# Kernel optimization log

Hardware: AMD Instinct MI355X
Metric: run time of the kernel (lower is better)

Reference implementation:

```python
import jax, jax.numpy as jnp
import numpy as np

B, H, W = 8, 64, 64
DIM_RGB, DIM_PL, EMBED, OUT = 256, 256, 128, 256
BN_EPS = 1e-5


def conv1x1(x, w, b=None):
    # x: (B,C,H,W), w: (D,C) -> (B,D,H,W)
    y = jnp.einsum('bchw,dc->bdhw', x, w)
    if b is not None:
        y = y + b[None, :, None, None]
    return y


def spatial_attention(q, k, v, scale):
    # q,k,v: (B,D,H,W)
    b, d, h, w = q.shape
    n = h * w
    qf = q.reshape(b, d, n).transpose(0, 2, 1)   # (B,N,D)
    kf = k.reshape(b, d, n)                       # (B,D,N)
    vf = v.reshape(b, d, n).transpose(0, 2, 1)   # (B,N,D)
    attn = jax.nn.softmax(jnp.einsum('bnd,bdm->bnm', qf, kf) * scale, axis=-1)
    out = jnp.einsum('bnm,bmd->bnd', attn, vf)   # (B,N,D)
    return out.transpose(0, 2, 1).reshape(b, d, h, w)


def setup_inputs() -> dict:
    key = jax.random.key(0)
    ks = jax.random.split(key, 20)
    s = 0.05
    inp = {
        'f_rgb': jax.random.normal(ks[0], (B, DIM_RGB, H, W), jnp.float32),
        'f_pl': jax.random.normal(ks[1], (B, DIM_PL, H, W), jnp.float32),
        'w_q_rgb': jax.random.normal(ks[2], (EMBED, DIM_RGB), jnp.float32) * s,
        'b_q_rgb': jax.random.normal(ks[3], (EMBED,), jnp.float32) * s,
        'w_k_pl': jax.random.normal(ks[4], (EMBED, DIM_PL), jnp.float32) * s,
        'b_k_pl': jax.random.normal(ks[5], (EMBED,), jnp.float32) * s,
        'w_v_pl': jax.random.normal(ks[6], (EMBED, DIM_PL), jnp.float32) * s,
        'b_v_pl': jax.random.normal(ks[7], (EMBED,), jnp.float32) * s,
        'w_q_pl': jax.random.normal(ks[8], (EMBED, DIM_PL), jnp.float32) * s,
        'b_q_pl': jax.random.normal(ks[9], (EMBED,), jnp.float32) * s,
        'w_k_rgb': jax.random.normal(ks[10], (EMBED, DIM_RGB), jnp.float32) * s,
        'b_k_rgb': jax.random.normal(ks[11], (EMBED,), jnp.float32) * s,
        'w_v_rgb': jax.random.normal(ks[12], (EMBED, DIM_RGB), jnp.float32) * s,
        'b_v_rgb': jax.random.normal(ks[13], (EMBED,), jnp.float32) * s,
        'w_proj': jax.random.normal(ks[14], (OUT, 2 * EMBED), jnp.float32) * s,
        'bn_gamma': jnp.ones((OUT,), jnp.float32),
        'bn_beta': jnp.zeros((OUT,), jnp.float32),
        'bn_mean': jax.random.normal(ks[15], (OUT,), jnp.float32) * 0.01,
        'bn_var': jax.random.uniform(ks[16], (OUT,), jnp.float32, 0.5, 1.5),
    }
    return inp


def reference(f_rgb, f_pl, w_q_rgb, b_q_rgb, w_k_pl, b_k_pl, w_v_pl, b_v_pl,
              w_q_pl, b_q_pl, w_k_rgb, b_k_rgb, w_v_rgb, b_v_rgb,
              w_proj, bn_gamma, bn_beta, bn_mean, bn_var):
    scale = EMBED ** -0.5
    out_rgb2pl = spatial_attention(
        conv1x1(f_rgb, w_q_rgb, b_q_rgb),
        conv1x1(f_pl, w_k_pl, b_k_pl),
        conv1x1(f_pl, w_v_pl, b_v_pl), scale)
    out_pl2rgb = spatial_attention(
        conv1x1(f_pl, w_q_pl, b_q_pl),
        conv1x1(f_rgb, w_k_rgb, b_k_rgb),
        conv1x1(f_rgb, w_v_rgb, b_v_rgb), scale)
    combined = jnp.concatenate([out_rgb2pl, out_pl2rgb], axis=1)  # (B,2E,H,W)
    y = conv1x1(combined, w_proj)  # no bias
    # BatchNorm2d (inference form) + ReLU
    inv = bn_gamma * jax.lax.rsqrt(bn_var + BN_EPS)
    y = y * inv[None, :, None, None] + (bn_beta - bn_mean * inv)[None, :, None, None]
    return jax.nn.relu(y)
```

## Files before the change

kernel.cpp:

```cpp
#include <hip/hip_runtime.h>
#include <hip/hip_bf16.h>
#include <hip/hip_fp16.h>

typedef _Float16 f16;
typedef _Float16 f16x8 __attribute__((ext_vector_type(8)));
typedef _Float16 f16x4 __attribute__((ext_vector_type(4)));
typedef __fp16 hf16x2 __attribute__((ext_vector_type(2)));
typedef float f32x4 __attribute__((ext_vector_type(4)));
typedef float f32x16 __attribute__((ext_vector_type(16)));

#define NP   4096
#define NB   8
#define CINC 256
#define EMB  128
#define OUTC 256
#define BN_EPS 1e-5f

#define DSZ  ((size_t)NB * NP * EMB)
#define TSZ  (2 * DSZ)

__global__ __launch_bounds__(256) void proj_all_kernel(
    const float* __restrict__ Xrgb, const float* __restrict__ Xpl,
    const float* __restrict__ w0, const float* __restrict__ b0,
    const float* __restrict__ w1, const float* __restrict__ b1,
    const float* __restrict__ w2, const float* __restrict__ b2,
    const float* __restrict__ w3, const float* __restrict__ b3,
    const float* __restrict__ w4, const float* __restrict__ b4,
    const float* __restrict__ w5, const float* __restrict__ b5,
    f16* __restrict__ Qt, f16* __restrict__ Kt, f16* __restrict__ Vn)
{
    const int m0 = blockIdx.x * 128;
    const int p  = blockIdx.y;
    const int b  = blockIdx.z;
    const int s  = (p >= 3) ? 1 : 0;
    const int j  = p - s * 3;
    const int tid = threadIdx.x;
    const int w = tid >> 6, lane = tid & 63, quad = lane >> 4, lr = lane & 15;

    const float* X  = s ? Xpl : Xrgb;
    const float* W  = p == 0 ? w0 : p == 1 ? w1 : p == 2 ? w2
                    : p == 3 ? w3 : p == 4 ? w4 : w5;
    const float* Bi = p == 0 ? b0 : p == 1 ? b1 : p == 2 ? b2
                    : p == 3 ? b3 : p == 4 ? b4 : b5;

    __shared__ __align__(16) f16 smem[128 * 72 * 2];
    f16* Al = smem;
    f16* Bl = smem + 128 * 72;

    f32x4 acc[2][8];
    #pragma unroll
    for (int mi = 0; mi < 2; ++mi)
        #pragma unroll
        for (int ni = 0; ni < 8; ++ni) acc[mi][ni] = (f32x4){0.f, 0.f, 0.f, 0.f};

    for (int kt = 0; kt < 4; ++kt) {
        const int kc0 = kt * 64;
        __syncthreads();
        for (int s2 = tid; s2 < 1024; s2 += 256) {
            const int n = s2 & 127, cg = s2 >> 7;
            f16 tmp[8];
            #pragma unroll
            for (int jj = 0; jj < 8; ++jj)
                tmp[jj] = (f16)X[((size_t)b * CINC + kc0 + cg * 8 + jj) * NP + m0 + n];
            *(f16x8*)&Al[n * 72 + cg * 8] = *(const f16x8*)tmp;
        }
        for (int s2 = tid; s2 < 1024; s2 += 256) {
            const int d = s2 >> 3, cg = s2 & 7;
            f16 tmp[8];
            #pragma unroll
            for (int jj = 0; jj < 8; ++jj)
                tmp[jj] = (f16)W[(size_t)d * CINC + kc0 + cg * 8 + jj];
            *(f16x8*)&Bl[d * 72 + cg * 8] = *(const f16x8*)tmp;
        }
        __syncthreads();
        #pragma unroll
        for (int ks = 0; ks < 2; ++ks) {
            f16x8 af[2], bfr[8];
            #pragma unroll
            for (int mi = 0; mi < 2; ++mi)
                af[mi] = *(const f16x8*)&Al[(w * 32 + mi * 16 + lr) * 72 + ks * 32 + quad * 8];
            #pragma unroll
            for (int ni = 0; ni < 8; ++ni)
                bfr[ni] = *(const f16x8*)&Bl[(ni * 16 + lr) * 72 + ks * 32 + quad * 8];
            #pragma unroll
            for (int mi = 0; mi < 2; ++mi)
                #pragma unroll
                for (int ni = 0; ni < 8; ++ni)
                    acc[mi][ni] = __builtin_amdgcn_mfma_f32_16x16x32_f16(
                        af[mi], bfr[ni], acc[mi][ni], 0, 0, 0);
        }
    }

    float bias[8];
    #pragma unroll
    for (int ni = 0; ni < 8; ++ni) bias[ni] = Bi[ni * 16 + lr];

    if (j < 2) {
        f16* out = (j == 0) ? (Qt + (size_t)s * DSZ) : (Kt + (size_t)(1 - s) * DSZ);
        #pragma unroll
        for (int mi = 0; mi < 2; ++mi)
            #pragma unroll
            for (int ni = 0; ni < 8; ++ni)
                #pragma unroll
                for (int r = 0; r < 4; ++r) {
                    const int n = m0 + w * 32 + mi * 16 + quad * 4 + r;
                    out[((size_t)b * NP + n) * EMB + ni * 16 + lr] =
                        (f16)(acc[mi][ni][r] + bias[ni]);
                }
    } else {
        f16* outV = Vn + (size_t)(1 - s) * DSZ;
        __syncthreads();
        f16* T = smem;
        const int quad_p = ((quad & 1) << 1) | (quad >> 1);
        #pragma unroll
        for (int mi = 0; mi < 2; ++mi)
            #pragma unroll
            for (int ni = 0; ni < 8; ++ni)
                #pragma unroll
                for (int r = 0; r < 4; ++r)
                    T[(ni * 16 + lr) * 136 + w * 32 + mi * 16 + quad_p * 4 + r] =
                        (f16)(acc[mi][ni][r] + bias[ni]);
        __syncthreads();
        for (int s2 = tid; s2 < 2048; s2 += 256) {
            const int d = s2 >> 4, n8 = (s2 & 15) * 8;
            *(f16x8*)&outV[((size_t)b * EMB + d) * NP + m0 + n8] =
                *(const f16x8*)&T[d * 136 + n8];
        }
    }
}

__global__ __launch_bounds__(256, 2) void attn_kernel(
    const f16* __restrict__ Qt, const f16* __restrict__ Kt,
    const f16* __restrict__ Vn, f16* __restrict__ combT)
{
    const int bid = blockIdx.x;
    const int g = bid & 15, dir = g >> 3, b = g & 7;
    const int n0 = (bid >> 4) * 128;
    const int tid = threadIdx.x;
    const int w = tid >> 6, lane = tid & 63;
    const int l31 = lane & 31, hi = lane >> 5;

    const f16* __restrict__ Q = Qt + ((size_t)dir * NB + b) * NP * EMB;
    const f16* __restrict__ K = Kt + ((size_t)dir * NB + b) * NP * EMB;
    const f16* __restrict__ V = Vn + ((size_t)dir * NB + b) * (size_t)EMB * NP;

    __shared__ __align__(16) f16 Kl[2][64 * 128];
    __shared__ __align__(16) f16 Vl[2][128 * 64];

    const int qbase = n0 + w * 32;

    f16x8 qf[8];
    #pragma unroll
    for (int d16 = 0; d16 < 8; ++d16) {
        f16x8 q = *(const f16x8*)&Q[(size_t)(qbase + l31) * EMB + d16 * 16 + hi * 8];
        #pragma unroll
        for (int jj = 0; jj < 8; ++jj)
            q[jj] = q[jj] * (f16)0.12752749f;
        qf[d16] = q;
    }

    f32x16 O[4];
    #pragma unroll
    for (int d32 = 0; d32 < 4; ++d32) O[d32] = (f32x16)(0.0f);
    float rs = 0.f;

    const int krp = lane >> 4, kp = lane & 15;
    const int vrp = lane >> 3, vp = lane & 7;
    f16x8 stK[4], stV[4];

    auto stage_load = [&](int m0) {
        #pragma unroll
        for (int i = 0; i < 4; ++i) {
            const int r = w * 16 + i * 4 + krp;
            const int c = kp ^ (r & 7);
            stK[i] = *(const f16x8*)&K[(size_t)(m0 + r) * EMB + c * 8];
        }
        #pragma unroll
        for (int i = 0; i < 4; ++i) {
            const int r = w * 32 + i * 8 + vrp;
            const int c = vp ^ (r & 7);
            stV[i] = *(const f16x8*)&V[(size_t)r * NP + m0 + c * 8];
        }
    };
    auto stage_write = [&](int buf) {
        #pragma unroll
        for (int i = 0; i < 4; ++i) {
            const int r = w * 16 + i * 4 + krp;
            *(f16x8*)&Kl[buf][r * 128 + kp * 8] = stK[i];
        }
        #pragma unroll
        for (int i = 0; i < 4; ++i) {
            const int r = w * 32 + i * 8 + vrp;
            *(f16x8*)&Vl[buf][r * 64 + vp * 8] = stV[i];
        }
    };

    stage_load(0);
    stage_write(0);
    int cur = 0;

    for (int t = 0; t < NP / 64; ++t) {
        __syncthreads();
        if (t < NP / 64 - 1) stage_load((t + 1) * 64);

        const f16* Kb = &Kl[cur][0];
        const f16* Vb = &Vl[cur][0];

        #pragma unroll
        for (int k32 = 0; k32 < 2; ++k32) {
            f32x16 s = (f32x16)(0.0f);
            __builtin_amdgcn_s_setprio(1);
            #pragma unroll
            for (int d16 = 0; d16 < 8; ++d16) {
                const int r = k32 * 32 + l31;
                const int c = (d16 * 2 + hi) ^ (r & 7);
                const f16x8 kf = *(const f16x8*)&Kb[r * 128 + c * 8];
                s = __builtin_amdgcn_mfma_f32_32x32x16_f16(kf, qf[d16], s, 0, 0, 0);
            }
            __builtin_amdgcn_s_setprio(0);

            float e[16];
            #pragma unroll
            for (int i = 0; i < 16; ++i) e[i] = __builtin_amdgcn_exp2f(s[i]);
            float sum = 0.f;
            #pragma unroll
            for (int i = 0; i < 16; ++i) sum += e[i];
            rs += sum;
            f16x8 pb[2];
            #pragma unroll
            for (int g2 = 0; g2 < 2; ++g2) {
                union { hf16x2 h[4]; f16x8 v; } pu;
                #pragma unroll
                for (int t2 = 0; t2 < 4; ++t2)
                    pu.h[t2] = __builtin_amdgcn_cvt_pkrtz(e[g2 * 8 + t2 * 2],
                                                          e[g2 * 8 + t2 * 2 + 1]);
                pb[g2] = pu.v;
            }

            __builtin_amdgcn_s_setprio(1);
            #pragma unroll
            for (int g2 = 0; g2 < 2; ++g2) {
                #pragma unroll
                for (int d32 = 0; d32 < 4; ++d32) {
                    const int r = d32 * 32 + l31;
                    const int c = (k32 * 4 + g2 * 2 + hi) ^ (r & 7);
                    const f16x8 vf = *(const f16x8*)&Vb[r * 64 + c * 8];
                    O[d32] = __builtin_amdgcn_mfma_f32_32x32x16_f16(vf, pb[g2], O[d32], 0, 0, 0);
                }
            }
            __builtin_amdgcn_s_setprio(0);
        }

        if (t < NP / 64 - 1) stage_write(cur ^ 1);
        cur ^= 1;
    }

    rs += __shfl_xor(rs, 32);
    const float inv = 1.0f / rs;
    const int n = qbase + l31;
    #pragma unroll
    for (int d32 = 0; d32 < 4; ++d32)
        #pragma unroll
        for (int tq = 0; tq < 4; ++tq) {
            f16 o4[4];
            #pragma unroll
            for (int jj = 0; jj < 4; ++jj)
                o4[jj] = (f16)(O[d32][tq * 4 + jj] * inv);
            *(f16x4*)&combT[((size_t)b * NP + n) * OUTC + dir * EMB + d32 * 32 + tq * 8 + hi * 4] =
                *(const f16x4*)o4;
        }
}

__global__ __launch_bounds__(256) void proj_out_kernel(
    const f16* __restrict__ combT, const float* __restrict__ Wp,
    const float* __restrict__ G, const float* __restrict__ Be,
    const float* __restrict__ Mu, const float* __restrict__ Va,
    float* __restrict__ out)
{
    const int m0 = blockIdx.x * 128;
    const int o0 = blockIdx.y * 128;
    const int b  = blockIdx.z;
    const int tid = threadIdx.x;
    const int w = tid >> 6, lane = tid & 63, quad = lane >> 4, lr = lane & 15;

    __shared__ __align__(16) f16 smem[128 * 72 * 2];
    f16* Al = smem;
    f16* Bl = smem + 128 * 72;

    f32x4 acc[2][8];
    #pragma unroll
    for (int mi = 0; mi < 2; ++mi)
        #pragma unroll
        for (int ni = 0; ni < 8; ++ni) acc[mi][ni] = (f32x4){0.f, 0.f, 0.f, 0.f};

    for (int kt = 0; kt < 4; ++kt) {
        const int kc0 = kt * 64;
        __syncthreads();
        #pragma unroll
        for (int i = 0; i < 4; ++i) {
            const int s2 = i * 256 + tid;
            const int n = s2 >> 3, cg = s2 & 7;
            *(f16x8*)&Al[n * 72 + cg * 8] =
                *(const f16x8*)&combT[((size_t)b * NP + m0 + n) * OUTC + kc0 + cg * 8];
        }
        for (int s2 = tid; s2 < 1024; s2 += 256) {
            const int d = s2 >> 3, cg = s2 & 7;
            f16 tmp[8];
            #pragma unroll
            for (int jj = 0; jj < 8; ++jj)
                tmp[jj] = (f16)Wp[(size_t)(o0 + d) * OUTC + kc0 + cg * 8 + jj];
            *(f16x8*)&Bl[d * 72 + cg * 8] = *(const f16x8*)tmp;
        }
        __syncthreads();
        #pragma unroll
        for (int ks = 0; ks < 2; ++ks) {
            f16x8 af[2], bfr[8];
            #pragma unroll
            for (int mi = 0; mi < 2; ++mi)
                af[mi] = *(const f16x8*)&Al[(w * 32 + mi * 16 + lr) * 72 + ks * 32 + quad * 8];
            #pragma unroll
            for (int ni = 0; ni < 8; ++ni)
                bfr[ni] = *(const f16x8*)&Bl[(ni * 16 + lr) * 72 + ks * 32 + quad * 8];
            #pragma unroll
            for (int mi = 0; mi < 2; ++mi)
                #pragma unroll
                for (int ni = 0; ni < 8; ++ni)
                    acc[mi][ni] = __builtin_amdgcn_mfma_f32_16x16x32_f16(
                        af[mi], bfr[ni], acc[mi][ni], 0, 0, 0);
        }
    }

    __syncthreads();
    f16* T = smem;
    #pragma unroll
    for (int ni = 0; ni < 8; ++ni) {
        const int o = o0 + ni * 16 + lr;
        const float iv = G[o] * rsqrtf(Va[o] + BN_EPS);
        const float sh = Be[o] - Mu[o] * iv;
        #pragma unroll
        for (int mi = 0; mi < 2; ++mi)
            #pragma unroll
            for (int r = 0; r < 4; ++r)
                T[(ni * 16 + lr) * 136 + w * 32 + mi * 16 + quad * 4 + r] =
                    (f16)fmaxf(acc[mi][ni][r] * iv + sh, 0.f);
    }
    __syncthreads();
    for (int s2 = tid; s2 < 2048; s2 += 256) {
        const int o = s2 >> 4, n8 = (s2 & 15) * 8;
        const f16x8 v = *(const f16x8*)&T[o * 136 + n8];
        const size_t off = ((size_t)b * OUTC + o0 + o) * NP + m0 + n8;
        #pragma unroll
        for (int k = 0; k < 8; ++k) out[off + k] = (float)v[k];
    }
}

extern "C" void kernel_launch(void* const* d_in, const int* in_sizes, int n_in,
                              void* d_out, int out_size, void* d_ws, size_t ws_size,
                              hipStream_t stream) {
    const float* f_rgb   = (const float*)d_in[0];
    const float* f_pl    = (const float*)d_in[1];
    const float* w_q_rgb = (const float*)d_in[2];  const float* b_q_rgb = (const float*)d_in[3];
    const float* w_k_pl  = (const float*)d_in[4];  const float* b_k_pl  = (const float*)d_in[5];
    const float* w_v_pl  = (const float*)d_in[6];  const float* b_v_pl  = (const float*)d_in[7];
    const float* w_q_pl  = (const float*)d_in[8];  const float* b_q_pl  = (const float*)d_in[9];
    const float* w_k_rgb = (const float*)d_in[10]; const float* b_k_rgb = (const float*)d_in[11];
    const float* w_v_rgb = (const float*)d_in[12]; const float* b_v_rgb = (const float*)d_in[13];
    const float* w_proj  = (const float*)d_in[14];
    const float* bn_g    = (const float*)d_in[15]; const float* bn_b = (const float*)d_in[16];
    const float* bn_m    = (const float*)d_in[17]; const float* bn_v = (const float*)d_in[18];

    f16* Qt    = (f16*)d_ws;
    f16* Kt    = Qt + TSZ;
    f16* Vn    = Kt + TSZ;
    f16* combT = Vn + TSZ;

    proj_all_kernel<<<dim3(32, 6, 8), 256, 0, stream>>>(
        f_rgb, f_pl,
        w_q_rgb, b_q_rgb, w_k_rgb, b_k_rgb, w_v_rgb, b_v_rgb,
        w_q_pl,  b_q_pl,  w_k_pl,  b_k_pl,  w_v_pl,  b_v_pl,
        Qt, Kt, Vn);

    attn_kernel<<<512, 256, 0, stream>>>(Qt, Kt, Vn, combT);

    proj_out_kernel<<<dim3(32, 2, 8), 256, 0, stream>>>(
        combT, w_proj, bn_g, bn_b, bn_m, bn_v, (float*)d_out);
}
```

Measured before the change: 347.5 us.

## Split attention over key halves and merge partials in output projection

Adds a split-K attention kernel. Each block handles 256 queries over half of the keys, with two 32-row query tiles per wave so every K fragment load feeds two MFMAs. Each block writes a normalized partial output plus its row sums, and the output projection kernel reweights and combines the two halves while loading its A tile. This raises register reuse of K/V loads and keeps the grid at 512 blocks. The cost is extra workspace, extra partial-output traffic, and a heavier A-load path in the projection kernel.

After: 754.7 us. 2.17x slower.

```diff
diff --git a/kernel.cpp b/kernel.cpp
--- a/kernel.cpp
+++ b/kernel.cpp
@@ -129,6 +129,168 @@
     }
 }
 
+__global__ __launch_bounds__(256, 2) void attn_split_kernel(
+    const f16* __restrict__ Qt, const f16* __restrict__ Kt,
+    const f16* __restrict__ Vn, f16* __restrict__ Op0,
+    f16* __restrict__ Op1, float* __restrict__ rsbuf)
+{
+    const int bid = blockIdx.x;
+    const int g = bid & 15, dir = g >> 3, b = g & 7;
+    const int nb = (bid >> 4) & 15;
+    const int kh = bid >> 8;
+    const int n0 = nb * 256;
+    const int m00 = kh * 2048;
+    const int tid = threadIdx.x;
+    const int w = tid >> 6, lane = tid & 63;
+    const int l31 = lane & 31, hi = lane >> 5;
+
+    const f16* __restrict__ Q = Qt + ((size_t)dir * NB + b) * NP * EMB;
+    const f16* __restrict__ K = Kt + ((size_t)dir * NB + b) * NP * EMB;
+    const f16* __restrict__ V = Vn + ((size_t)dir * NB + b) * (size_t)EMB * NP;
+    f16* __restrict__ Op = kh ? Op1 : Op0;
+    float* __restrict__ rsp = rsbuf + (size_t)kh * 2 * NB * NP + ((size_t)dir * NB + b) * NP;
+
+    __shared__ __align__(16) f16 Kl[2][64 * 128];
+    __shared__ __align__(16) f16 Vl[2][128 * 64];
+
+    const int qbase = n0 + w * 64;
+
+    f16x8 qf[2][8];
+    #pragma unroll
+    for (int q32 = 0; q32 < 2; ++q32)
+        #pragma unroll
+        for (int d16 = 0; d16 < 8; ++d16) {
+            f16x8 q = *(const f16x8*)&Q[(size_t)(qbase + q32 * 32 + l31) * EMB + d16 * 16 + hi * 8];
+            #pragma unroll
+            for (int jj = 0; jj < 8; ++jj)
+                q[jj] = q[jj] * (f16)0.12752749f;
+            qf[q32][d16] = q;
+        }
+
+    f32x16 O[4][2];
+    #pragma unroll
+    for (int d32 = 0; d32 < 4; ++d32)
+        #pragma unroll
+        for (int q32 = 0; q32 < 2; ++q32) O[d32][q32] = (f32x16)(0.0f);
+    float rs[2] = {0.f, 0.f};
+
+    const int krp = lane >> 4, kp = lane & 15;
+    const int vrp = lane >> 3, vp = lane & 7;
+    f16x8 stK[4], stV[4];
+
+    auto stage_load = [&](int mm) {
+        #pragma unroll
+        for (int i = 0; i < 4; ++i) {
+            const int r = w * 16 + i * 4 + krp;
+            const int c = kp ^ (r & 7);
+            stK[i] = *(const f16x8*)&K[(size_t)(mm + r) * EMB + c * 8];
+        }
+        #pragma unroll
+        for (int i = 0; i < 4; ++i) {
+            const int r = w * 32 + i * 8 + vrp;
+            const int c = vp ^ (r & 7);
+            stV[i] = *(const f16x8*)&V[(size_t)r * NP + mm + c * 8];
+        }
+    };
+    auto stage_write = [&](int buf) {
+        #pragma unroll
+        for (int i = 0; i < 4; ++i) {
+            const int r = w * 16 + i * 4 + krp;
+            *(f16x8*)&Kl[buf][r * 128 + kp * 8] = stK[i];
+        }
+        #pragma unroll
+        for (int i = 0; i < 4; ++i) {
+            const int r = w * 32 + i * 8 + vrp;
+            *(f16x8*)&Vl[buf][r * 64 + vp * 8] = stV[i];
+        }
+    };
+
+    stage_load(m00);
+    stage_write(0);
+    int cur = 0;
+
+    for (int t = 0; t < 32; ++t) {
+        __syncthreads();
+        if (t < 31) stage_load(m00 + (t + 1) * 64);
+
+        const f16* Kb = &Kl[cur][0];
+        const f16* Vb = &Vl[cur][0];
+
+        #pragma unroll
+        for (int k32 = 0; k32 < 2; ++k32) {
+            f32x16 s0 = (f32x16)(0.0f), s1 = (f32x16)(0.0f);
+            __builtin_amdgcn_s_setprio(1);
+            #pragma unroll
+            for (int d16 = 0; d16 < 8; ++d16) {
+                const int r = k32 * 32 + l31;
+                const int c = (d16 * 2 + hi) ^ (r & 7);
+                const f16x8 kf = *(const f16x8*)&Kb[r * 128 + c * 8];
+                s0 = __builtin_amdgcn_mfma_f32_32x32x16_f16(kf, qf[0][d16], s0, 0, 0, 0);
+                s1 = __builtin_amdgcn_mfma_f32_32x32x16_f16(kf, qf[1][d16], s1, 0, 0, 0);
+            }
+            __builtin_amdgcn_s_setprio(0);
+
+            f16x8 pb[2][2];
+            #pragma unroll
+            for (int q32 = 0; q32 < 2; ++q32) {
+                const f32x16 s = q32 ? s1 : s0;
+                float e[16];
+                #pragma unroll
+                for (int i = 0; i < 16; ++i) e[i] = __builtin_amdgcn_exp2f(s[i]);
+                float sum = 0.f;
+                #pragma unroll
+                for (int i = 0; i < 16; ++i) sum += e[i];
+                rs[q32] += sum;
+                #pragma unroll
+                for (int g2 = 0; g2 < 2; ++g2) {
+                    union { hf16x2 h[4]; f16x8 v; } pu;
+                    #pragma unroll
+                    for (int t2 = 0; t2 < 4; ++t2)
+                        pu.h[t2] = __builtin_amdgcn_cvt_pkrtz(e[g2 * 8 + t2 * 2],
+                                                              e[g2 * 8 + t2 * 2 + 1]);
+                    pb[g2][q32] = pu.v;
+                }
+            }
+
+            __builtin_amdgcn_s_setprio(1);
+            #pragma unroll
+            for (int g2 = 0; g2 < 2; ++g2) {
+                #pragma unroll
+                for (int d32 = 0; d32 < 4; ++d32) {
+                    const int r = d32 * 32 + l31;
+                    const int c = (k32 * 4 + g2 * 2 + hi) ^ (r & 7);
+                    const f16x8 vf = *(const f16x8*)&Vb[r * 64 + c * 8];
+                    O[d32][0] = __builtin_amdgcn_mfma_f32_32x32x16_f16(vf, pb[g2][0], O[d32][0], 0, 0, 0);
+                    O[d32][1] = __builtin_amdgcn_mfma_f32_32x32x16_f16(vf, pb[g2][1], O[d32][1], 0, 0, 0);
+                }
+            }
+            __builtin_amdgcn_s_setprio(0);
+        }
+
+        if (t < 31) stage_write(cur ^ 1);
+        cur ^= 1;
+    }
+
+    #pragma unroll
+    for (int q32 = 0; q32 < 2; ++q32) {
+        rs[q32] += __shfl_xor(rs[q32], 32);
+        const float inv = 1.0f / rs[q32];
+        const int n = qbase + q32 * 32 + l31;
+        #pragma unroll
+        for (int d32 = 0; d32 < 4; ++d32)
+            #pragma unroll
+            for (int tq = 0; tq < 4; ++tq) {
+                f16 o4[4];
+                #pragma unroll
+                for (int jj = 0; jj < 4; ++jj)
+                    o4[jj] = (f16)(O[d32][q32][tq * 4 + jj] * inv);
+                *(f16x4*)&Op[((size_t)b * NP + n) * OUTC + dir * EMB + d32 * 32 + tq * 8 + hi * 4] =
+                    *(const f16x4*)o4;
+            }
+        if (hi == 0) rsp[n] = rs[q32];
+    }
+}
+
 __global__ __launch_bounds__(256, 2) void attn_kernel(
     const f16* __restrict__ Qt, const f16* __restrict__ Kt,
     const f16* __restrict__ Vn, f16* __restrict__ combT)
@@ -271,8 +433,10 @@
         }
 }
 
+template <int COMBINE>
 __global__ __launch_bounds__(256) void proj_out_kernel(
-    const f16* __restrict__ combT, const float* __restrict__ Wp,
+    const f16* __restrict__ Ap0, const f16* __restrict__ Ap1,
+    const float* __restrict__ rsbuf, const float* __restrict__ Wp,
     const float* __restrict__ G, const float* __restrict__ Be,
     const float* __restrict__ Mu, const float* __restrict__ Va,
     float* __restrict__ out)
@@ -296,12 +460,32 @@
     for (int kt = 0; kt < 4; ++kt) {
         const int kc0 = kt * 64;
         __syncthreads();
-        #pragma unroll
-        for (int i = 0; i < 4; ++i) {
-            const int s2 = i * 256 + tid;
-            const int n = s2 >> 3, cg = s2 & 7;
-            *(f16x8*)&Al[n * 72 + cg * 8] =
-                *(const f16x8*)&combT[((size_t)b * NP + m0 + n) * OUTC + kc0 + cg * 8];
+        if (COMBINE) {
+            const int dirc = kt >> 1;
+            for (int s2 = tid; s2 < 1024; s2 += 256) {
+                const int n = s2 >> 3, cg = s2 & 7;
+                const size_t off = ((size_t)b * NP + m0 + n) * OUTC + kc0 + cg * 8;
+                const f16x8 a0 = *(const f16x8*)&Ap0[off];
+                const f16x8 a1 = *(const f16x8*)&Ap1[off];
+                const size_t ri = ((size_t)dirc * NB + b) * NP + m0 + n;
+                const float r0 = rsbuf[ri];
+                const float r1 = rsbuf[(size_t)2 * NB * NP + ri];
+                const float wt = 1.0f / (r0 + r1);
+                const float w0 = r0 * wt, w1 = r1 * wt;
+                f16 tmp[8];
+                #pragma unroll
+                for (int jj = 0; jj < 8; ++jj)
+                    tmp[jj] = (f16)(w0 * (float)a0[jj] + w1 * (float)a1[jj]);
+                *(f16x8*)&Al[n * 72 + cg * 8] = *(const f16x8*)tmp;
+            }
+        } else {
+            #pragma unroll
+            for (int i = 0; i < 4; ++i) {
+                const int s2 = i * 256 + tid;
+                const int n = s2 >> 3, cg = s2 & 7;
+                *(f16x8*)&Al[n * 72 + cg * 8] =
+                    *(const f16x8*)&Ap0[((size_t)b * NP + m0 + n) * OUTC + kc0 + cg * 8];
+            }
         }
         for (int s2 = tid; s2 < 1024; s2 += 256) {
             const int d = s2 >> 3, cg = s2 & 7;
@@ -369,10 +553,9 @@
     const float* bn_g    = (const float*)d_in[15]; const float* bn_b = (const float*)d_in[16];
     const float* bn_m    = (const float*)d_in[17]; const float* bn_v = (const float*)d_in[18];
 
-    f16* Qt    = (f16*)d_ws;
-    f16* Kt    = Qt + TSZ;
-    f16* Vn    = Kt + TSZ;
-    f16* combT = Vn + TSZ;
+    f16* Qt = (f16*)d_ws;
+    f16* Kt = Qt + TSZ;
+    f16* Vn = Kt + TSZ;
 
     proj_all_kernel<<<dim3(32, 6, 8), 256, 0, stream>>>(
         f_rgb, f_pl,
@@ -380,8 +563,18 @@
         w_q_pl,  b_q_pl,  w_k_pl,  b_k_pl,  w_v_pl,  b_v_pl,
         Qt, Kt, Vn);
 
-    attn_kernel<<<512, 256, 0, stream>>>(Qt, Kt, Vn, combT);
-
-    proj_out_kernel<<<dim3(32, 2, 8), 256, 0, stream>>>(
-        combT, w_proj, bn_g, bn_b, bn_m, bn_v, (float*)d_out);
+    const size_t NEED = (size_t)5 * TSZ * sizeof(f16) + (size_t)4 * NB * NP * sizeof(float);
+    if (ws_size >= NEED) {
+        f16*  Op0   = Vn + TSZ;
+        f16*  Op1   = Op0 + TSZ;
+        float* rsbuf = (float*)(Op1 + TSZ);
+        attn_split_kernel<<<512, 256, 0, stream>>>(Qt, Kt, Vn, Op0, Op1, rsbuf);
+        proj_out_kernel<1><<<dim3(32, 2, 8), 256, 0, stream>>>(
+            Op0, Op1, rsbuf, w_proj, bn_g, bn_b, bn_m, bn_v, (float*)d_out);
+    } else {
+        f16* combT = Vn + TSZ;
+        attn_kernel<<<512, 256, 0, stream>>>(Qt, Kt, Vn, combT);
+        proj_out_kernel<0><<<dim3(32, 2, 8), 256, 0, stream>>>(
+            combT, combT, (const float*)combT, w_proj, bn_g, bn_b, bn_m, bn_v, (float*)d_out);
+    }
 }
```
